# Kernel tuning notes

Hardware: AMD Instinct MI355X
Metric: run time of the kernel (lower is better)

## Reference

```python
import jax, jax.numpy as jnp
import numpy as np

B, L, D = 2, 2048, 2048
H, KV = 32, 8
HD = D // H          # 64
REP = H // KV        # 4


def setup_inputs() -> dict:
    key = jax.random.key(0)
    ks = jax.random.split(key, 6)
    x = jax.random.normal(ks[0], (B, L, D), dtype=jnp.float32)
    # weights stored [in, out] (transpose of torch Linear weight), scaled for stability
    wq = jax.random.normal(ks[1], (D, H * HD), dtype=jnp.float32) * 0.02
    wk = jax.random.normal(ks[2], (D, KV * HD), dtype=jnp.float32) * 0.02
    wv = jax.random.normal(ks[3], (D, KV * HD), dtype=jnp.float32) * 0.02
    wo = jax.random.normal(ks[4], (H * HD, D), dtype=jnp.float32) * 0.02
    # RoPE frequencies: freqs_cis = exp(i * pos * theta), theta_j = 10000^{-2j/HD}
    inv_freq = 1.0 / (10000.0 ** (jnp.arange(0, HD, 2, dtype=jnp.float32) / HD))  # [HD/2]
    angles = jnp.arange(L, dtype=jnp.float32)[:, None] * inv_freq[None, :]        # [L, HD/2]
    freqs_cos = jnp.cos(angles)
    freqs_sin = jnp.sin(angles)
    # additive causal mask [L, L] (prefill from start_pos=0)
    mask = jnp.where(jnp.tril(jnp.ones((L, L), dtype=bool)), 0.0, -jnp.inf).astype(jnp.float32)
    return {"x": x, "start_pos": 0, "freqs_cos": freqs_cos, "freqs_sin": freqs_sin,
            "mask": mask, "wq": wq, "wk": wk, "wv": wv, "wo": wo}


def _apply_rope(t, cos, sin):
    # t: [B, L, h, HD]; cos/sin: [L, HD/2] -> broadcast [1, L, 1, HD/2]
    tp = t.reshape(*t.shape[:-1], HD // 2, 2)
    a, b = tp[..., 0], tp[..., 1]
    c = cos[None, :, None, :]
    s = sin[None, :, None, :]
    ra = a * c - b * s
    rb = a * s + b * c
    return jnp.stack([ra, rb], axis=-1).reshape(t.shape)


def reference(x, start_pos, freqs_cos, freqs_sin, mask, wq, wk, wv, wo):
    xq = jnp.einsum('bld,de->ble', x, wq).reshape(B, L, H, HD)
    xk = jnp.einsum('bld,de->ble', x, wk).reshape(B, L, KV, HD)
    xv = jnp.einsum('bld,de->ble', x, wv).reshape(B, L, KV, HD)
    xq = _apply_rope(xq, freqs_cos, freqs_sin)
    xk = _apply_rope(xk, freqs_cos, freqs_sin)
    # (cache write of xk/xv is a dead side effect in the torch module; omitted)
    # GQA: query head (g*REP + r) attends to kv head g  == repeat_interleave semantics
    q = xq.transpose(0, 2, 1, 3).reshape(B, KV, REP, L, HD)  # [B,KV,REP,L,HD]
    k = xk.transpose(0, 2, 1, 3)                              # [B,KV,L,HD]
    v = xv.transpose(0, 2, 1, 3)
    scale = 1.0 / jnp.sqrt(jnp.float32(HD))
    scores = jnp.einsum('bgrld,bgmd->bgrlm', q, k) * scale + mask  # [B,KV,REP,L,L]
    attn = jax.nn.softmax(scores, axis=-1)
    out = jnp.einsum('bgrlm,bgmd->bgrld', attn, v)            # [B,KV,REP,L,HD]
    out = out.reshape(B, H, L, HD).transpose(0, 2, 1, 3).reshape(B, L, H * HD)
    return jnp.einsum('ble,ed->bld', out, wo)
```

## Files before the change

### kernel.cpp

```cpp
#include <hip/hip_runtime.h>
#include <hip/hip_bf16.h>
#include <math.h>

typedef __bf16 bf16_t;
typedef __bf16 bf16x8 __attribute__((ext_vector_type(8)));
typedef __bf16 bf16x4 __attribute__((ext_vector_type(4)));
typedef __bf16 bf16x2 __attribute__((ext_vector_type(2)));
typedef float  f32x4  __attribute__((ext_vector_type(4)));
typedef int    i32x4  __attribute__((ext_vector_type(4)));

#define B_  2
#define L_  2048
#define D_  2048
#define H_  32
#define KV_ 8
#define HD_ 64

static __device__ __forceinline__ void gload_lds16(const bf16_t* g, void* l)
{
    __builtin_amdgcn_global_load_lds(
        (const __attribute__((address_space(1))) void*)g,
        (__attribute__((address_space(3))) void*)l, 16, 0, 0);
}

static __device__ __forceinline__ int packbf(float a, float b)
{
    bf16x2 t; t[0] = (bf16_t)a; t[1] = (bf16_t)b;
    return __builtin_bit_cast(int, t);
}

static __device__ __forceinline__ void pl32(int& a, int& b)
{
    asm("v_permlane32_swap_b32 %0, %1" : "+v"(a), "+v"(b));
}
static __device__ __forceinline__ void pl16(int& a, int& b)
{
    asm("v_permlane16_swap_b32 %0, %1" : "+v"(a), "+v"(b));
}

#define WAITV8() asm volatile("s_waitcnt vmcnt(8)" ::: "memory")
#define WAITV4() asm volatile("s_waitcnt vmcnt(4)" ::: "memory")
#define WAITV0() asm volatile("s_waitcnt vmcnt(0)" ::: "memory")
#define WAITL0() asm volatile("s_waitcnt lgkmcnt(0)" ::: "memory")

__global__ void cast_f32_bf16(const float4* __restrict__ in,
                              bf16x4* __restrict__ out, int n4)
{
    const int i = blockIdx.x * 256 + threadIdx.x;
    if (i >= n4) return;
    const float4 v = in[i];
    bf16x4 o;
    o[0] = (bf16_t)v.x; o[1] = (bf16_t)v.y; o[2] = (bf16_t)v.z; o[3] = (bf16_t)v.w;
    out[i] = o;
}

template <typename InT>
__global__ void transpose_cast(const InT* __restrict__ in, bf16_t* __restrict__ out,
                               int R, int C)
{
    __shared__ bf16_t tile[32][33];
    const int bx = blockIdx.x * 32, by = blockIdx.y * 32;
    in  += (size_t)blockIdx.z * R * C;
    out += (size_t)blockIdx.z * R * C;
    const int tx = threadIdx.x, ty = threadIdx.y;
#pragma unroll
    for (int i = ty; i < 32; i += 8)
        tile[i][tx] = (bf16_t)(float)in[(size_t)(by + i) * C + bx + tx];
    __syncthreads();
#pragma unroll
    for (int i = ty; i < 32; i += 8)
        out[(size_t)(bx + i) * R + by + tx] = tile[tx][i];
}

template <typename OutT>
__global__ __launch_bounds__(256) void gemm_tn(
    const bf16_t* __restrict__ A,
    const bf16_t* __restrict__ BT,
    OutT* __restrict__ C,
    int M, int N, int K)
{
    __shared__ __attribute__((aligned(16))) bf16_t As[128 * 32];
    __shared__ __attribute__((aligned(16))) bf16_t Bs[128 * 32];

    const int m0   = blockIdx.y * 128;
    const int n0   = blockIdx.x * 128;
    const int tid  = threadIdx.x;
    const int wave = tid >> 6;
    const int lane = tid & 63;
    const int quad = lane >> 4;
    const int l16  = lane & 15;
    const int wm   = (wave & 1) * 64;
    const int wn   = (wave >> 1) * 64;
    const int sr   = tid >> 2;
    const int sc   = (tid & 3) * 8;

    f32x4 acc[4][4];
    const f32x4 zf = {0.f, 0.f, 0.f, 0.f};
#pragma unroll
    for (int i = 0; i < 4; i++)
#pragma unroll
        for (int j = 0; j < 4; j++) acc[i][j] = zf;

    const bf16_t* ag = A  + (size_t)(m0 + sr) * K + sc;
    const bf16_t* bg = BT + (size_t)(n0 + sr) * K + sc;
    bf16_t* asl = As + tid * 8;
    bf16_t* bsl = Bs + tid * 8;

    for (int k0 = 0; k0 < K; k0 += 32) {
        gload_lds16(ag + k0,                  asl);
        gload_lds16(ag + (size_t)64 * K + k0, asl + 2048);
        gload_lds16(bg + k0,                  bsl);
        gload_lds16(bg + (size_t)64 * K + k0, bsl + 2048);
        __syncthreads();

        bf16x8 af[4], bfr[4];
#pragma unroll
        for (int i = 0; i < 4; i++)
            af[i] = *(const bf16x8*)(&As[(wm + i * 16 + l16) * 32 + quad * 8]);
#pragma unroll
        for (int i = 0; i < 4; i++)
            bfr[i] = *(const bf16x8*)(&Bs[(wn + i * 16 + l16) * 32 + quad * 8]);

#pragma unroll
        for (int mi = 0; mi < 4; mi++)
#pragma unroll
            for (int ni = 0; ni < 4; ni++)
                acc[mi][ni] = __builtin_amdgcn_mfma_f32_16x16x32_bf16(
                    af[mi], bfr[ni], acc[mi][ni], 0, 0, 0);
        __syncthreads();
    }

#pragma unroll
    for (int mi = 0; mi < 4; mi++)
#pragma unroll
        for (int ni = 0; ni < 4; ni++)
#pragma unroll
            for (int r = 0; r < 4; r++) {
                const int row = m0 + wm + mi * 16 + quad * 4 + r;
                const int col = n0 + wn + ni * 16 + l16;
                C[(size_t)row * N + col] = (OutT)acc[mi][ni][r];
            }
}

#define FRAG(base, row, kk) \
    (*(const bf16x8*)((base) + (size_t)(row) * 128 + ((((kk) * 4 + quad) ^ sw8) << 4)))

#define STG_A(kt, h, buf) do {                                                        \
    gload_lds16(Ag + (size_t)((h) * 128)      * 2048 + (size_t)(kt) * 64,             \
                sdst + (buf) * 32768 + (h) * 16384);                                  \
    gload_lds16(Ag + (size_t)((h) * 128 + 64) * 2048 + (size_t)(kt) * 64,             \
                sdst + (buf) * 32768 + (h) * 16384 + 8192);                           \
} while (0)

#define STG_B(kt, h, buf) do {                                                        \
    gload_lds16(Bg + (size_t)((h) * 128)      * 2048 + (size_t)(kt) * 64,             \
                sdst + 65536 + (buf) * 32768 + (h) * 16384);                          \
    gload_lds16(Bg + (size_t)((h) * 128 + 64) * 2048 + (size_t)(kt) * 64,             \
                sdst + 65536 + (buf) * 32768 + (h) * 16384 + 8192);                   \
} while (0)

#define PHASE_SET(AB, BB, STG1, STG2, STG3, STG4, VM4)                                \
  {                                        \
    _Pragma("unroll") for (int m = 0; m < 4; m++) {                                   \
        Afr[m][0] = FRAG(AB, arow + m * 16, 0);                                       \
        Afr[m][1] = FRAG(AB, arow + m * 16, 1); }                                     \
    _Pragma("unroll") for (int n = 0; n < 2; n++) {                                   \
        B01[n][0] = FRAG(BB, brow + n * 16, 0);                                       \
        B01[n][1] = FRAG(BB, brow + n * 16, 1); }                                     \
    STG1;                                                                             \
    asm volatile("s_waitcnt lgkmcnt(8)" ::: "memory");                                \
    __builtin_amdgcn_s_barrier();                                                     \
    WAITL0();                                                                         \
    __builtin_amdgcn_s_setprio(1);                                                    \
    _Pragma("unroll") for (int m = 0; m < 4; m++)                                     \
      _Pragma("unroll") for (int n = 0; n < 2; n++)                                   \
        _Pragma("unroll") for (int kk = 0; kk < 2; kk++)                              \
          acc[m][n] = __builtin_amdgcn_mfma_f32_16x16x32_bf16(                        \
              Afr[m][kk], B01[n][kk], acc[m][n], 0, 0, 0);                            \
    __builtin_amdgcn_s_setprio(0);                                                    \
    __builtin_amdgcn_s_barrier();                                                     \
  }                                                                                   \
  {                                                 \
    _Pragma("unroll") for (int n = 0; n < 2; n++) {                                   \
        B23[n][0] = FRAG(BB, brow + (n + 2) * 16, 0);                                 \
        B23[n][1] = FRAG(BB, brow + (n + 2) * 16, 1); }                               \
    STG2;                                                                             \
    __builtin_amdgcn_s_barrier();                                                     \
    WAITL0();                                                                         \
    __builtin_amdgcn_s_setprio(1);                                                    \
    _Pragma("unroll") for (int m = 0; m < 4; m++)                                     \
      _Pragma("unroll") for (int n = 0; n < 2; n++)                                   \
        _Pragma("unroll") for (int kk = 0; kk < 2; kk++)                              \
          acc[m][n + 2] = __builtin_amdgcn_mfma_f32_16x16x32_bf16(                    \
              Afr[m][kk], B23[n][kk], acc[m][n + 2], 0, 0, 0);                        \
    __builtin_amdgcn_s_setprio(0);                                                    \
    __builtin_amdgcn_s_barrier();                                                     \
  }                                                                                   \
  {                                                 \
    _Pragma("unroll") for (int m = 0; m < 4; m++) {                                   \
        Afr[m][0] = FRAG(AB, arow + (m + 4) * 16, 0);                                 \
        Afr[m][1] = FRAG(AB, arow + (m + 4) * 16, 1); }                               \
    STG3;                                                                             \
    __builtin_amdgcn_s_barrier();                                                     \
    WAITL0();                                                                         \
    __builtin_amdgcn_s_setprio(1);                                                    \
    _Pragma("unroll") for (int m = 0; m < 4; m++)                                     \
      _Pragma("unroll") for (int n = 0; n < 2; n++)                                   \
        _Pragma("unroll") for (int kk = 0; kk < 2; kk++)                              \
          acc[m + 4][n + 2] = __builtin_amdgcn_mfma_f32_16x16x32_bf16(                \
              Afr[m][kk], B23[n][kk], acc[m + 4][n + 2], 0, 0, 0);                    \
    __builtin_amdgcn_s_setprio(0);                                                    \
    __builtin_amdgcn_s_barrier();                                                     \
  }                                                                                   \
  {                                        \
    STG4;                                                                             \
    VM4;                                                                              \
    __builtin_amdgcn_s_barrier();                                                     \
    __builtin_amdgcn_s_setprio(1);                                                    \
    _Pragma("unroll") for (int m = 0; m < 4; m++)                                     \
      _Pragma("unroll") for (int n = 0; n < 2; n++)                                   \
        _Pragma("unroll") for (int kk = 0; kk < 2; kk++)                              \
          acc[m + 4][n] = __builtin_amdgcn_mfma_f32_16x16x32_bf16(                    \
              Afr[m][kk], B01[n][kk], acc[m + 4][n], 0, 0, 0);                        \
    __builtin_amdgcn_s_setprio(0);                                                    \
    __builtin_amdgcn_s_barrier();                                                     \
  }

__global__ __launch_bounds__(512, 2) void gemm_qkv(
    const bf16_t* __restrict__ A,
    const bf16_t* __restrict__ BT,
    bf16_t* __restrict__ Qb, bf16_t* __restrict__ Kb, bf16_t* __restrict__ Vb)
{
    extern __shared__ __attribute__((aligned(16))) char DLDS[];
    constexpr int NITER = 2048 / 64 / 2;

    const int tid  = threadIdx.x;
    const int wave = tid >> 6;
    const int lane = tid & 63;
    const int quad = lane >> 4;
    const int l16  = lane & 15;
    const int wr   = wave >> 2;
    const int wc   = wave & 3;
    const int m0   = blockIdx.y * 256;
    const int n0   = blockIdx.x * 256;

    const int srow  = tid >> 3;
    const int swcol = ((tid & 7) ^ (srow & 7)) * 8;
    const bf16_t* Ag = A  + (size_t)(m0 + srow) * 2048 + swcol;
    const bf16_t* Bg = BT + (size_t)(n0 + srow) * 2048 + swcol;
    char* sdst = DLDS + tid * 16;

    const char* AB0 = DLDS;
    const char* AB1 = DLDS + 32768;
    const char* BB0 = DLDS + 65536;
    const char* BB1 = DLDS + 98304;
    const int sw8  = l16 & 7;
    const int arow = wr * 128 + l16;
    const int brow = wc * 64 + l16;

    f32x4 acc[8][4];
    const f32x4 zf = {0.f, 0.f, 0.f, 0.f};
#pragma unroll
    for (int i = 0; i < 8; i++)
#pragma unroll
        for (int j = 0; j < 4; j++) acc[i][j] = zf;

    bf16x8 Afr[4][2], B01[2][2], B23[2][2];

    STG_B(0, 0, 0); STG_B(0, 1, 0); STG_A(0, 0, 0); STG_A(0, 1, 0);
    STG_B(1, 0, 1); STG_B(1, 1, 1);
    WAITV4();
    __builtin_amdgcn_s_barrier();

    for (int i = 0; i < NITER; ++i) {
        const int t1 = 2 * i + 1;
        const int t2 = 2 * i + 2;
        const int t3 = 2 * i + 3;
        const bool more = (i + 1 < NITER);

        PHASE_SET(AB0, BB0,
                  STG_A(t1, 0, 1),
                  STG_A(t1, 1, 1),
                  if (more) STG_B(t2, 0, 0),
                  if (more) STG_B(t2, 1, 0),
                  if (more) { WAITV4(); } else { WAITV0(); })
        PHASE_SET(AB1, BB1,
                  if (more) STG_A(t2, 0, 0),
                  if (more) STG_A(t2, 1, 0),
                  if (more) STG_B(t3, 0, 1),
                  if (more) STG_B(t3, 1, 1),
                  WAITV4())
    }

    bf16_t* Cb; int ldc, coff; float cs = 1.f;
    if (n0 < 2048)      { Cb = Qb; ldc = 2048; coff = 0; }
    else if (n0 < 2560) { Cb = Kb; ldc = 512;  coff = 2048;
                          cs = 0.18033688011112042f; }
    else                { Cb = Vb; ldc = 512;  coff = 2560; }

#pragma unroll
    for (int mt = 0; mt < 8; mt++)
#pragma unroll
        for (int nt = 0; nt < 4; nt++)
#pragma unroll
            for (int r = 0; r < 4; r++) {
                const int row = m0 + wr * 128 + mt * 16 + quad * 4 + r;
                const int col = n0 + wc * 64 + nt * 16 + l16 - coff;
                Cb[(size_t)row * ldc + col] = (bf16_t)(acc[mt][nt][r] * cs);
            }
}

#undef FRAG
#undef STG_A
#undef STG_B
#undef PHASE_SET

__global__ void rope_k(bf16_t* __restrict__ T, const float* __restrict__ fc,
                       const float* __restrict__ fs, int nheads, int total8)
{
    const int idx = blockIdx.x * 256 + threadIdx.x;
    if (idx >= total8) return;
    const int g  = idx & 7;
    const int t  = idx >> 3;
    const int h  = t % nheads;
    const int bl = t / nheads;
    const int l  = bl & (L_ - 1);
    const float4 c4 = *(const float4*)(fc + l * 32 + g * 4);
    const float4 s4 = *(const float4*)(fs + l * 32 + g * 4);
    const size_t off = ((size_t)bl * nheads + h) * 64 + g * 8;
    const bf16x8 v = *(const bf16x8*)(T + off);
    const float cc[4] = {c4.x, c4.y, c4.z, c4.w};
    const float ss[4] = {s4.x, s4.y, s4.z, s4.w};
    bf16x8 o;
#pragma unroll
    for (int p = 0; p < 4; p++) {
        const float a  = (float)v[2 * p];
        const float b2 = (float)v[2 * p + 1];
        o[2 * p]     = (bf16_t)(a * cc[p] - b2 * ss[p]);
        o[2 * p + 1] = (bf16_t)(a * ss[p] + b2 * cc[p]);
    }
    *(bf16x8*)(T + off) = o;
}

__global__ __launch_bounds__(256, 2) void attn_k(
    const bf16_t* __restrict__ Q,
    const bf16_t* __restrict__ Kc,
    const bf16_t* __restrict__ VT,
    bf16_t* __restrict__ Ob)
{
    __shared__ __attribute__((aligned(16))) char LDS[65536];
    float* OL = (float*)LDS;
    float* LR = (float*)(LDS + 17408);

    const int tid  = threadIdx.x;
    const int wave = tid >> 6;
    const int lane = tid & 63;
    const int quad = lane >> 4;
    const int l16  = lane & 15;

    const int id   = blockIdx.y * 16 + blockIdx.x;
    const int c    = (id >> 3) & 15;
    const int bh   = (id & 7) * 8 + (id >> 7);
    const int bb   = bh >> 5;
    const int h    = bh & 31;
    const int kvh  = h >> 2;
    const size_t bbL = (size_t)bb * L_;

    const int schunk = ((lane & 3) ^ ((lane >> 3) & 3)) * 8;
    const int sw16   = ((l16 >> 1) & 3) * 16;

    const bf16_t* Kg = Kc + bbL * (KV_ * HD_) + kvh * HD_;
    const bf16_t* Vg = VT + (size_t)(bb * KV_ + kvh) * HD_ * L_;
    const bf16_t* KgL = Kg + (size_t)(wave * 32 + (lane >> 2)) * (KV_ * HD_) + schunk;
    const bf16_t* VgL = Vg + (size_t)(lane >> 2) * L_ + wave * 32 + schunk;
    char* kdst0 = (char*)LDS + wave * 2048 + (lane << 4);
    char* vdst0 = (char*)LDS + 16384 + wave * 4096 + (lane << 4);

    const f32x4 zf = {0.f, 0.f, 0.f, 0.f};

    for (int half = 0; half < 2; ++half) {
        const int j     = half ? c : 31 - c;
        const int qbase = j * 64;
        const int nkt   = (j + 2) >> 1;

        bf16x8 qf[4][2];
#pragma unroll
        for (int qt = 0; qt < 4; qt++) {
            const bf16_t* qrow = Q + ((bbL + qbase + qt * 16 + l16) * H_ + h) * HD_;
            qf[qt][0] = *(const bf16x8*)(qrow + quad * 8);
            qf[qt][1] = *(const bf16x8*)(qrow + 32 + quad * 8);
        }

        f32x4 acc[4][4];
#pragma unroll
        for (int mt = 0; mt < 4; mt++)
#pragma unroll
            for (int qt = 0; qt < 4; qt++) acc[mt][qt] = zf;
        float lacc[4] = {0.f, 0.f, 0.f, 0.f};

        {
            const int ktb = 0;
#pragma unroll
            for (int cc = 0; cc < 2; cc++)
#pragma unroll
                for (int sub = 0; sub < 2; sub++)
                    gload_lds16(KgL + (size_t)(ktb + sub * 16) * (KV_ * HD_) + cc * 32,
                                kdst0 + cc * 8192 + sub * 1024);
#pragma unroll
            for (int sub = 0; sub < 4; sub++)
                gload_lds16(VgL + (size_t)(sub * 16) * L_ + ktb,
                            vdst0 + sub * 1024);
        }

        for (int kt = 0; kt < nkt; kt++) {
            if (kt + 1 < nkt) {
                WAITL0();
                const int d = ((kt + 1) & 1) * 32768;
                const int ktb = (kt + 1) * 128;
#pragma unroll
                for (int cc = 0; cc < 2; cc++)
#pragma unroll
                    for (int sub = 0; sub < 2; sub++)
                        gload_lds16(KgL + (size_t)(ktb + sub * 16) * (KV_ * HD_) + cc * 32,
                                    kdst0 + d + cc * 8192 + sub * 1024);
#pragma unroll
                for (int sub = 0; sub < 4; sub++)
                    gload_lds16(VgL + (size_t)(sub * 16) * L_ + ktb,
                                vdst0 + d + sub * 1024);
                WAITV8();
            } else {
                WAITV0();
            }

            const char* Kld = LDS + (kt & 1) * 32768;
            const char* Vld = Kld + 16384;

            bf16x8 kf[2][2];
#pragma unroll
            for (int t = 0; t < 2; t++)
#pragma unroll
                for (int cc = 0; cc < 2; cc++)
                    kf[t][cc] = *(const bf16x8*)(Kld + cc * 8192 +
                        (wave * 32 + t * 16 + l16) * 64 + ((quad * 16) ^ sw16));

            bf16x8 vf[4];
#pragma unroll
            for (int mt = 0; mt < 4; mt++)
                vf[mt] = *(const bf16x8*)(Vld + wave * 4096 +
                    (mt * 16 + l16) * 64 + ((quad * 16) ^ sw16));

            f32x4 st[2][4];
            __builtin_amdgcn_s_setprio(1);
#pragma unroll
            for (int t = 0; t < 2; t++)
#pragma unroll
                for (int qt = 0; qt < 4; qt++) {
                    f32x4 s = __builtin_amdgcn_mfma_f32_16x16x32_bf16(
                        kf[t][0], qf[qt][0], zf, 0, 0, 0);
                    st[t][qt] = __builtin_amdgcn_mfma_f32_16x16x32_bf16(
                        kf[t][1], qf[qt][1], s, 0, 0, 0);
                }
            __builtin_amdgcn_s_setprio(0);

            if (kt == nkt - 1) {
                const int kq = kt * 128 + wave * 32 + quad * 4 - qbase - l16;
#pragma unroll
                for (int t = 0; t < 2; t++)
#pragma unroll
                    for (int qt = 0; qt < 4; qt++)
#pragma unroll
                        for (int r = 0; r < 4; r++)
                            st[t][qt][r] = (kq + t * 16 - qt * 16 + r <= 0)
                                         ? st[t][qt][r] : -__builtin_inff();
            }

            int pk[2][4][2];
#pragma unroll
            for (int t = 0; t < 2; t++)
#pragma unroll
                for (int qt = 0; qt < 4; qt++) {
                    const float e0 = __builtin_amdgcn_exp2f(st[t][qt][0]);
                    const float e1 = __builtin_amdgcn_exp2f(st[t][qt][1]);
                    const float e2 = __builtin_amdgcn_exp2f(st[t][qt][2]);
                    const float e3 = __builtin_amdgcn_exp2f(st[t][qt][3]);
                    lacc[qt] += (e0 + e1) + (e2 + e3);
                    pk[t][qt][0] = packbf(e0, e1);
                    pk[t][qt][1] = packbf(e2, e3);
                }

#pragma unroll
            for (int qt = 0; qt < 4; qt++) {
                int a0 = pk[0][qt][0], b0 = pk[1][qt][0];
                pl32(a0, b0); pl16(a0, b0);
                int a1 = pk[0][qt][1], b1 = pk[1][qt][1];
                pl32(a1, b1); pl16(a1, b1);
                i32x4 bi;
                bi[0] = a0; bi[1] = a1; bi[2] = b0; bi[3] = b1;
                const bf16x8 pb = __builtin_bit_cast(bf16x8, bi);
                __builtin_amdgcn_s_setprio(1);
#pragma unroll
                for (int mt = 0; mt < 4; mt++)
                    acc[mt][qt] = __builtin_amdgcn_mfma_f32_16x16x32_bf16(
                        vf[mt], pb, acc[mt][qt], 0, 0, 0);
                __builtin_amdgcn_s_setprio(0);
            }
        }

        float lw[4];
#pragma unroll
        for (int qt = 0; qt < 4; qt++) {
            float v = lacc[qt];
            v += __shfl_xor(v, 16);
            v += __shfl_xor(v, 32);
            lw[qt] = v;
        }

        __syncthreads();

        if (quad == 0)
#pragma unroll
            for (int qt = 0; qt < 4; qt++)
                LR[(wave * 4 + qt) * 16 + l16] = lw[qt];

#pragma unroll
        for (int p = 0; p < 4; p++) {
#pragma unroll
            for (int qt = 0; qt < 4; qt++) {
                if (((qt - wave) & 3) == p) {
#pragma unroll
                    for (int mt = 0; mt < 4; mt++) {
                        float* a = OL + (qt * 16 + l16) * 68 + mt * 16 + quad * 4;
                        if (p == 0) *(f32x4*)a = acc[mt][qt];
                        else        *(f32x4*)a = *(f32x4*)a + acc[mt][qt];
                    }
                }
            }
            __syncthreads();
        }

        const float ls = LR[(0 * 4 + wave) * 16 + l16] + LR[(1 * 4 + wave) * 16 + l16]
                       + LR[(2 * 4 + wave) * 16 + l16] + LR[(3 * 4 + wave) * 16 + l16];
        const float inv = 1.f / ls;
        bf16_t* orow = Ob + ((bbL + qbase + wave * 16 + l16) * H_ + h) * HD_;
#pragma unroll
        for (int j2 = 0; j2 < 4; j2++) {
            const f32x4 v = *(const f32x4*)(OL + (wave * 16 + l16) * 68 + quad * 16 + j2 * 4);
            bf16x4 o;
#pragma unroll
            for (int i = 0; i < 4; i++) o[i] = (bf16_t)(v[i] * inv);
            *(bf16x4*)(orow + quad * 16 + j2 * 4) = o;
        }
        __syncthreads();
    }
}

extern "C" void kernel_launch(void* const* d_in, const int* in_sizes, int n_in,
                              void* d_out, int out_size, void* d_ws, size_t ws_size,
                              hipStream_t stream)
{
    (void)in_sizes; (void)n_in; (void)out_size; (void)ws_size;
    const float* xf = (const float*)d_in[0];
    const float* fc = (const float*)d_in[2];
    const float* fs = (const float*)d_in[3];
    const float* wq = (const float*)d_in[5];
    const float* wk = (const float*)d_in[6];
    const float* wv = (const float*)d_in[7];
    const float* wo = (const float*)d_in[8];
    float* out = (float*)d_out;

    char* ws = (char*)d_ws;
    bf16_t* xb   = (bf16_t*)(ws);
    bf16_t* Qb   = (bf16_t*)(ws + (16ull << 20));
    bf16_t* Kb   = (bf16_t*)(ws + (32ull << 20));
    bf16_t* Vb   = (bf16_t*)(ws + (36ull << 20));
    bf16_t* VTb  = (bf16_t*)(ws + (40ull << 20));
    bf16_t* Oa   = (bf16_t*)(ws + (44ull << 20));
    bf16_t* Wqkv = (bf16_t*)(ws + (60ull << 20));
    bf16_t* WoT  = (bf16_t*)(ws + (72ull << 20));

    cast_f32_bf16<<<8192, 256, 0, stream>>>((const float4*)xf, (bf16x4*)xb,
                                            B_ * L_ * D_ / 4);

    const dim3 tb(32, 8);
    transpose_cast<float><<<dim3(64, 64, 1), tb, 0, stream>>>(wq, Wqkv, 2048, 2048);
    transpose_cast<float><<<dim3(16, 64, 1), tb, 0, stream>>>(wk, Wqkv + 2048ull * 2048, 2048, 512);
    transpose_cast<float><<<dim3(16, 64, 1), tb, 0, stream>>>(wv, Wqkv + 2560ull * 2048, 2048, 512);
    transpose_cast<float><<<dim3(64, 64, 1), tb, 0, stream>>>(wo, WoT, 2048, 2048);

    gemm_qkv<<<dim3(12, 16), 512, 131072, stream>>>(xb, Wqkv, Qb, Kb, Vb);

    rope_k<<<4096, 256, 0, stream>>>(Qb, fc, fs, 32, B_ * L_ * 32 * 8);
    rope_k<<<1024, 256, 0, stream>>>(Kb, fc, fs, 8, B_ * L_ * 8 * 8);

    transpose_cast<bf16_t><<<dim3(16, 64, 2), tb, 0, stream>>>(Vb, VTb, 2048, 512);

    attn_k<<<dim3(16, 64), 256, 0, stream>>>(Qb, Kb, VTb, Oa);

    gemm_tn<float><<<dim3(16, 32), 256, 0, stream>>>(Oa, WoT, out, 4096, 2048, 2048);
}
```

Measured before the change: 330.2 us.

## Replace output projection GEMM with double-buffered swizzled 256x128 tile kernel

Replaces the simple 128x128 single-buffered output-projection GEMM with a 512-thread kernel that computes 256x128 tiles. It double-buffers 64-wide K slices in swizzled LDS, issues direct global-to-LDS loads interleaved with MFMA phases, and raises wave priority around the MFMA blocks. The block index is remapped so neighbouring blocks share A/B panels. The goal is to hide global load latency, avoid LDS bank conflicts and improve reuse. In exchange the kernel uses more LDS and more registers per block, and the fine-grained barrier and waitcnt scheduling must be correct.

```diff
diff --git a/kernel.cpp b/kernel.cpp
--- a/kernel.cpp
+++ b/kernel.cpp
@@ -40,6 +40,7 @@
 
 #define WAITV8() asm volatile("s_waitcnt vmcnt(8)" ::: "memory")
 #define WAITV4() asm volatile("s_waitcnt vmcnt(4)" ::: "memory")
+#define WAITV2() asm volatile("s_waitcnt vmcnt(2)" ::: "memory")
 #define WAITV0() asm volatile("s_waitcnt vmcnt(0)" ::: "memory")
 #define WAITL0() asm volatile("s_waitcnt lgkmcnt(0)" ::: "memory")
 
@@ -70,76 +71,6 @@
 #pragma unroll
     for (int i = ty; i < 32; i += 8)
         out[(size_t)(bx + i) * R + by + tx] = tile[tx][i];
-}
-
-template <typename OutT>
-__global__ __launch_bounds__(256) void gemm_tn(
-    const bf16_t* __restrict__ A,
-    const bf16_t* __restrict__ BT,
-    OutT* __restrict__ C,
-    int M, int N, int K)
-{
-    __shared__ __attribute__((aligned(16))) bf16_t As[128 * 32];
-    __shared__ __attribute__((aligned(16))) bf16_t Bs[128 * 32];
-
-    const int m0   = blockIdx.y * 128;
-    const int n0   = blockIdx.x * 128;
-    const int tid  = threadIdx.x;
-    const int wave = tid >> 6;
-    const int lane = tid & 63;
-    const int quad = lane >> 4;
-    const int l16  = lane & 15;
-    const int wm   = (wave & 1) * 64;
-    const int wn   = (wave >> 1) * 64;
-    const int sr   = tid >> 2;
-    const int sc   = (tid & 3) * 8;
-
-    f32x4 acc[4][4];
-    const f32x4 zf = {0.f, 0.f, 0.f, 0.f};
-#pragma unroll
-    for (int i = 0; i < 4; i++)
-#pragma unroll
-        for (int j = 0; j < 4; j++) acc[i][j] = zf;
-
-    const bf16_t* ag = A  + (size_t)(m0 + sr) * K + sc;
-    const bf16_t* bg = BT + (size_t)(n0 + sr) * K + sc;
-    bf16_t* asl = As + tid * 8;
-    bf16_t* bsl = Bs + tid * 8;
-
-    for (int k0 = 0; k0 < K; k0 += 32) {
-        gload_lds16(ag + k0,                  asl);
-        gload_lds16(ag + (size_t)64 * K + k0, asl + 2048);
-        gload_lds16(bg + k0,                  bsl);
-        gload_lds16(bg + (size_t)64 * K + k0, bsl + 2048);
-        __syncthreads();
-
-        bf16x8 af[4], bfr[4];
-#pragma unroll
-        for (int i = 0; i < 4; i++)
-            af[i] = *(const bf16x8*)(&As[(wm + i * 16 + l16) * 32 + quad * 8]);
-#pragma unroll
-        for (int i = 0; i < 4; i++)
-            bfr[i] = *(const bf16x8*)(&Bs[(wn + i * 16 + l16) * 32 + quad * 8]);
-
-#pragma unroll
-        for (int mi = 0; mi < 4; mi++)
-#pragma unroll
-            for (int ni = 0; ni < 4; ni++)
-                acc[mi][ni] = __builtin_amdgcn_mfma_f32_16x16x32_bf16(
-                    af[mi], bfr[ni], acc[mi][ni], 0, 0, 0);
-        __syncthreads();
-    }
-
-#pragma unroll
-    for (int mi = 0; mi < 4; mi++)
-#pragma unroll
-        for (int ni = 0; ni < 4; ni++)
-#pragma unroll
-            for (int r = 0; r < 4; r++) {
-                const int row = m0 + wm + mi * 16 + quad * 4 + r;
-                const int col = n0 + wn + ni * 16 + l16;
-                C[(size_t)row * N + col] = (OutT)acc[mi][ni][r];
-            }
 }
 
 #define FRAG(base, row, kk) \
@@ -314,6 +245,142 @@
 #undef STG_A
 #undef STG_B
 #undef PHASE_SET
+
+#define OFRAG(base, row, kk) \
+    (*(const bf16x8*)((base) + (size_t)(row) * 128 + ((((kk) * 4 + quad) ^ sw8) << 4)))
+
+#define OSTG_A(kt, h, buf) do {                                                       \
+    gload_lds16(Ag + (size_t)((h) * 128)      * 2048 + (size_t)(kt) * 64,             \
+                adst + (buf) * 32768 + (h) * 16384);                                  \
+    gload_lds16(Ag + (size_t)((h) * 128 + 64) * 2048 + (size_t)(kt) * 64,             \
+                adst + (buf) * 32768 + (h) * 16384 + 8192);                           \
+} while (0)
+
+#define OSTG_B(kt, buf) do {                                                          \
+    gload_lds16(Bg + (size_t)(kt) * 64,                       bdst + (buf) * 16384);  \
+    gload_lds16(Bg + (size_t)64 * 2048 + (size_t)(kt) * 64,   bdst + (buf) * 16384 + 8192); \
+} while (0)
+
+#define OTILE(AB, BB, SA, SB, VMW)                                                    \
+  {                                             \
+    _Pragma("unroll") for (int m = 0; m < 4; m++) {                                   \
+        Afr[m][0] = OFRAG(AB, arow + m * 16, 0);                                      \
+        Afr[m][1] = OFRAG(AB, arow + m * 16, 1); }                                    \
+    _Pragma("unroll") for (int n = 0; n < 2; n++) {                                   \
+        Bfr[n][0] = OFRAG(BB, brow + n * 16, 0);                                      \
+        Bfr[n][1] = OFRAG(BB, brow + n * 16, 1); }                                    \
+    SA;                                                                               \
+    asm volatile("s_waitcnt lgkmcnt(8)" ::: "memory");                                \
+    __builtin_amdgcn_s_barrier();                                                     \
+    WAITL0();                                                                         \
+    __builtin_amdgcn_s_setprio(1);                                                    \
+    _Pragma("unroll") for (int m = 0; m < 4; m++)                                     \
+      _Pragma("unroll") for (int n = 0; n < 2; n++)                                   \
+        _Pragma("unroll") for (int kk = 0; kk < 2; kk++)                              \
+          acc[m][n] = __builtin_amdgcn_mfma_f32_16x16x32_bf16(                        \
+              Afr[m][kk], Bfr[n][kk], acc[m][n], 0, 0, 0);                            \
+    __builtin_amdgcn_s_setprio(0);                                                    \
+    __builtin_amdgcn_s_barrier();                                                     \
+  }                                                                                   \
+  {                                \
+    _Pragma("unroll") for (int m = 0; m < 4; m++) {                                   \
+        Afr[m][0] = OFRAG(AB, arow + (m + 4) * 16, 0);                                \
+        Afr[m][1] = OFRAG(AB, arow + (m + 4) * 16, 1); }                              \
+    SB;                                                                               \
+    VMW;                                                                              \
+    __builtin_amdgcn_s_barrier();                                                     \
+    WAITL0();                                                                         \
+    __builtin_amdgcn_s_setprio(1);                                                    \
+    _Pragma("unroll") for (int m = 0; m < 4; m++)                                     \
+      _Pragma("unroll") for (int n = 0; n < 2; n++)                                   \
+        _Pragma("unroll") for (int kk = 0; kk < 2; kk++)                              \
+          acc[m + 4][n] = __builtin_amdgcn_mfma_f32_16x16x32_bf16(                    \
+              Afr[m][kk], Bfr[n][kk], acc[m + 4][n], 0, 0, 0);                        \
+    __builtin_amdgcn_s_setprio(0);                                                    \
+    __builtin_amdgcn_s_barrier();                                                     \
+  }
+
+__global__ __launch_bounds__(512, 2) void gemm_out(
+    const bf16_t* __restrict__ A,
+    const bf16_t* __restrict__ BT,
+    float* __restrict__ C)
+{
+    extern __shared__ __attribute__((aligned(16))) char DLDS[];
+    constexpr int NITER = 2048 / 64 / 2;
+
+    const int tid  = threadIdx.x;
+    const int wave = tid >> 6;
+    const int lane = tid & 63;
+    const int quad = lane >> 4;
+    const int l16  = lane & 15;
+    const int wr   = wave >> 2;
+    const int wc   = wave & 3;
+
+    const int id   = blockIdx.x;
+    const int w    = id >> 3;
+    const int m0   = ((id & 7) * 2 + (w & 1)) * 256;
+    const int n0   = (w >> 1) * 128;
+
+    const int srow  = tid >> 3;
+    const int swcol = ((tid & 7) ^ (srow & 7)) * 8;
+    const bf16_t* Ag = A  + (size_t)(m0 + srow) * 2048 + swcol;
+    const bf16_t* Bg = BT + (size_t)(n0 + srow) * 2048 + swcol;
+    char* adst = DLDS + tid * 16;
+    char* bdst = DLDS + 65536 + tid * 16;
+
+    const char* AB0 = DLDS;
+    const char* AB1 = DLDS + 32768;
+    const char* BB0 = DLDS + 65536;
+    const char* BB1 = DLDS + 81920;
+    const int sw8  = l16 & 7;
+    const int arow = wr * 128 + l16;
+    const int brow = wc * 32 + l16;
+
+    f32x4 acc[8][2];
+    const f32x4 zf = {0.f, 0.f, 0.f, 0.f};
+#pragma unroll
+    for (int i = 0; i < 8; i++)
+#pragma unroll
+        for (int j = 0; j < 2; j++) acc[i][j] = zf;
+
+    bf16x8 Afr[4][2], Bfr[2][2];
+
+    OSTG_B(0, 0); OSTG_A(0, 0, 0); OSTG_A(0, 1, 0); OSTG_B(1, 1);
+    WAITV2();
+    __builtin_amdgcn_s_barrier();
+
+    for (int i = 0; i < NITER; ++i) {
+        const int v  = 2 * i + 1;
+        const int t2 = 2 * i + 2;
+        const int t3 = 2 * i + 3;
+        const bool more = (i + 1 < NITER);
+
+        OTILE(AB0, BB0,
+              { OSTG_A(v, 0, 1); OSTG_A(v, 1, 1); },
+              { if (more) OSTG_B(t2, 0); },
+              if (more) { WAITV2(); } else { WAITV0(); })
+        OTILE(AB1, BB1,
+              { if (more) { OSTG_A(t2, 0, 0); OSTG_A(t2, 1, 0); } },
+              { if (more) OSTG_B(t3, 1); },
+              if (more) { WAITV2(); } else { WAITV0(); })
+    }
+
+#pragma unroll
+    for (int mt = 0; mt < 8; mt++)
+#pragma unroll
+        for (int nt = 0; nt < 2; nt++)
+#pragma unroll
+            for (int r = 0; r < 4; r++) {
+                const int row = m0 + wr * 128 + mt * 16 + quad * 4 + r;
+                const int col = n0 + wc * 32 + nt * 16 + l16;
+                C[(size_t)row * 2048 + col] = acc[mt][nt][r];
+            }
+}
+
+#undef OFRAG
+#undef OSTG_A
+#undef OSTG_B
+#undef OTILE
 
 __global__ void rope_k(bf16_t* __restrict__ T, const float* __restrict__ fc,
                        const float* __restrict__ fs, int nheads, int total8)
@@ -596,5 +663,5 @@
 
     attn_k<<<dim3(16, 64), 256, 0, stream>>>(Qb, Kb, VTb, Oa);
 
-    gemm_tn<float><<<dim3(16, 32), 256, 0, stream>>>(Oa, WoT, out, 4096, 2048, 2048);
-}
+    gemm_out<<<dim3(256), 512, 98304, stream>>>(Oa, WoT, out);
+}
```

New measurement: 308.0 us. 1.07x faster.
